# Optimization experiments

Measured on AMD Instinct MI355X. Metric: run time of the kernel, lower is better.

Reference implementation:

```python
import jax, jax.numpy as jnp
import numpy as np

N = 50000          # nodes
F = 128            # feature dim (indim = outdim)
AVG_DEG = 12       # random edges per node (plus one self-loop)
AVG_D_LOG = 2.6    # avg_d['log'] used by PNA scalers
EPS = 1e-5         # PNA std epsilon / BatchNorm eps


def setup_inputs() -> dict:
    key = jax.random.key(0)
    k1, k2, k3, k4 = jax.random.split(key, 4)
    h = jax.random.normal(k1, (N, F), dtype=jnp.float32)
    E_rand = N * AVG_DEG
    src_r = jax.random.randint(k2, (E_rand,), 0, N)
    dst_r = jax.random.randint(k3, (E_rand,), 0, N)
    loop = jnp.arange(N)
    src = jnp.concatenate([src_r, loop]).astype(jnp.int64) if jax.config.jax_enable_x64 else jnp.concatenate([src_r, loop]).astype(jnp.int32)
    dst = jnp.concatenate([dst_r, loop]).astype(src.dtype)
    concat_dim = F * (1 + 4 * 3)  # indim * (1 + n_aggr * n_scalers)
    W = jax.random.normal(k4, (concat_dim, F), dtype=jnp.float32) * (1.0 / np.sqrt(concat_dim))
    b = jnp.zeros((F,), dtype=jnp.float32)
    gamma = jnp.ones((F,), dtype=jnp.float32)
    beta = jnp.zeros((F,), dtype=jnp.float32)
    return {"h": h, "src": src, "dst": dst, "W": W, "b": b, "gamma": gamma, "beta": beta}


def _pna_forward(h, W, b, gamma, beta, src, dst):
    n = h.shape[0]
    m = h[src]                                            # [E, F] gathered mailbox
    deg = jax.ops.segment_sum(jnp.ones(src.shape[0], h.dtype), dst, num_segments=n)
    deg = jnp.maximum(deg, 1.0)[:, None]                  # every node has a self-loop
    s = jax.ops.segment_sum(m, dst, num_segments=n)
    mean = s / deg
    mx = jax.ops.segment_max(m, dst, num_segments=n)
    mn = jax.ops.segment_min(m, dst, num_segments=n)
    mean_sq = jax.ops.segment_sum(m * m, dst, num_segments=n) / deg
    std = jnp.sqrt(jax.nn.relu(mean_sq - mean * mean) + EPS)
    agg = jnp.concatenate([mean, mx, mn, std], axis=1)    # [N, 4F]
    logd = jnp.log(deg + 1.0)                             # [N, 1]
    scaled = jnp.concatenate([agg,
                              agg * (logd / AVG_D_LOG),
                              agg * (AVG_D_LOG / logd)], axis=1)  # [N, 12F]
    hc = jnp.concatenate([h, scaled], axis=1)             # [N, 13F]
    out = hc @ W + b                                      # posttrans (single linear)
    out = jax.nn.relu(out)                                # activation (dropout p=0)
    mu = out.mean(axis=0)                                 # BatchNorm1d, training stats
    var = out.var(axis=0)                                 # biased variance (torch)
    out = gamma * (out - mu) * jax.lax.rsqrt(var + EPS) + beta
    return out


def reference(h, src, dst, W, b, gamma, beta):
    return _pna_forward(h, W, b, gamma, beta, src, dst)
```

## Files before the change

kernel.cpp:

```cpp
#include <hip/hip_runtime.h>
#include <math.h>

#define FDIM 128
#define AVG_D_LOGF 2.6f
#define BN_EPS 1e-5f
#define NK5 5

using f32x2 = __attribute__((ext_vector_type(2))) float;
using f32x4 = __attribute__((ext_vector_type(4))) float;
using s16x8 = __attribute__((ext_vector_type(8))) short;
using u16x8 = __attribute__((ext_vector_type(8))) unsigned short;

__device__ __forceinline__ unsigned short f2bf(float x) {
  unsigned int u = __float_as_uint(x);
  u += 0x7FFFu + ((u >> 16) & 1u);
  return (unsigned short)(u >> 16);
}
__device__ __forceinline__ f32x2 bfpair(unsigned int u) {
  union { uint2 u2; f32x2 f; } c;
  c.u2 = make_uint2(u << 16, u & 0xFFFF0000u);
  return c.f;
}
__device__ __forceinline__ void gload16(const void* g, void* l) {
  __builtin_amdgcn_global_load_lds(
      (const __attribute__((address_space(1))) void*)g,
      (__attribute__((address_space(3))) void*)l, 16, 0, 0);
}

__global__ void prep_kernel(const float* __restrict__ h, unsigned short* __restrict__ hb,
                            const float* __restrict__ W, unsigned short* __restrict__ wBT,
                            const int* __restrict__ dst, int* __restrict__ deg,
                            int w0, int w1, int w2, int K) {
  int i = blockIdx.x * 256 + threadIdx.x;
  if (i < w0) {
    const f32x4* sp = (const f32x4*)h + (size_t)i * 2;
    f32x4 v0 = sp[0], v1 = sp[1];
    u16x8 o;
    o[0] = f2bf(v0[0]); o[1] = f2bf(v0[1]); o[2] = f2bf(v0[2]); o[3] = f2bf(v0[3]);
    o[4] = f2bf(v1[0]); o[5] = f2bf(v1[1]); o[6] = f2bf(v1[2]); o[7] = f2bf(v1[3]);
    *((u16x8*)hb + i) = o;
  } else if (i < w0 + w1) {
    int idx = i - w0;
    int k = idx >> 7, j = idx & 127;
    wBT[(size_t)j * K + k] = f2bf(W[idx]);
  } else if (i < w0 + w1 + w2) {
    atomicAdd(&deg[dst[i - w0 - w1]], 1);
  }
}

__global__ void scan1(const int* __restrict__ deg, int* __restrict__ offs,
                      int* __restrict__ bsums, int n) {
  __shared__ int tmp[256];
  int t = threadIdx.x, i = blockIdx.x * 256 + t;
  int v = (i < n) ? deg[i] : 0;
  tmp[t] = v; __syncthreads();
  for (int d = 1; d < 256; d <<= 1) {
    int x = (t >= d) ? tmp[t - d] : 0;
    __syncthreads();
    tmp[t] += x;
    __syncthreads();
  }
  if (i < n) offs[i] = tmp[t] - v;
  if (t == 255) bsums[blockIdx.x] = tmp[255];
}

__global__ void csr_fill(const int* __restrict__ src, const int* __restrict__ dst,
                         const int* __restrict__ offs, const int* __restrict__ bsums,
                         int* __restrict__ cursor, int* __restrict__ csr, int E, int nb) {
  __shared__ int tmp[256];
  __shared__ int ex[256];
  const int t = threadIdx.x;
  {
    int v = (t < nb) ? bsums[t] : 0;
    tmp[t] = v; __syncthreads();
    for (int d = 1; d < 256; d <<= 1) {
      int x = (t >= d) ? tmp[t - d] : 0;
      __syncthreads();
      tmp[t] += x;
      __syncthreads();
    }
    ex[t] = tmp[t] - v;
    __syncthreads();
  }
  int i = blockIdx.x * 256 + t;
  if (i < E) {
    int d = dst[i];
    int pos = offs[d] + ex[d >> 8] + atomicAdd(&cursor[d], 1);
    csr[pos] = src[i] << 8;
  }
}

__global__ __launch_bounds__(256) void agg_kernel(
    const unsigned short* __restrict__ hb, const int* __restrict__ csr,
    const int* __restrict__ offs, const int* __restrict__ bsums,
    unsigned short* __restrict__ aggb, float2* __restrict__ s12a,
    int n, int E, int nb) {
  __shared__ int tmp[256];
  __shared__ int ex[256];
  {
    int t = threadIdx.x;
    int v = (t < nb) ? bsums[t] : 0;
    tmp[t] = v; __syncthreads();
    for (int d = 1; d < 256; d <<= 1) {
      int x = (t >= d) ? tmp[t - d] : 0;
      __syncthreads();
      tmp[t] += x;
      __syncthreads();
    }
    ex[t] = tmp[t] - v;
    __syncthreads();
  }
  const int gw = (blockIdx.x * 256 + threadIdx.x) >> 6;
  const int lane = threadIdx.x & 63;
  if (gw >= n) return;
  const int beg = offs[gw] + ex[gw >> 8];
  const int end = (gw + 1 < n) ? offs[gw + 1] + ex[(gw + 1) >> 8] : E;
  const int sub = lane >> 5;
  const int fl  = lane & 31;
  const char* hbase = (const char*)hb + fl * 8;

  f32x2 s0v = {0.f, 0.f}, s1v = {0.f, 0.f};
  f32x2 q0v = {0.f, 0.f}, q1v = {0.f, 0.f};
  f32x2 mx0 = {-INFINITY, -INFINITY}, mx1 = {-INFINITY, -INFINITY};
  f32x2 mn0 = {INFINITY, INFINITY},  mn1 = {INFINITY, INFINITY};

  auto acc1 = [&](uint2 A) {
    f32x2 a0 = bfpair(A.x), a1 = bfpair(A.y);
    s0v += a0; s1v += a1;
    q0v += a0 * a0; q1v += a1 * a1;
    mx0[0] = fmaxf(mx0[0], a0[0]); mx0[1] = fmaxf(mx0[1], a0[1]);
    mx1[0] = fmaxf(mx1[0], a1[0]); mx1[1] = fmaxf(mx1[1], a1[1]);
    mn0[0] = fminf(mn0[0], a0[0]); mn0[1] = fminf(mn0[1], a0[1]);
    mn1[0] = fminf(mn1[0], a1[0]); mn1[1] = fminf(mn1[1], a1[1]);
  };
  auto gat = [&](int byteoff) -> uint2 {
    return *(const uint2*)(hbase + byteoff);
  };

  const int cnt = end - beg;
  const int pairs = cnt >> 1;
  int p = 0;
  for (; p + 4 <= pairs; p += 4) {
    int base = beg + 2 * p + sub;
    int i0 = csr[base], i1 = csr[base + 2], i2 = csr[base + 4], i3 = csr[base + 6];
    uint2 A = gat(i0), B = gat(i1), C = gat(i2), D = gat(i3);
    acc1(A); acc1(B); acc1(C); acc1(D);
  }
  for (; p < pairs; ++p) {
    acc1(gat(csr[beg + 2 * p + sub]));
  }
  if ((cnt & 1) && sub == 0) {
    acc1(gat(csr[end - 1]));
  }

  s0v[0] += __shfl_xor(s0v[0], 32); s0v[1] += __shfl_xor(s0v[1], 32);
  s1v[0] += __shfl_xor(s1v[0], 32); s1v[1] += __shfl_xor(s1v[1], 32);
  q0v[0] += __shfl_xor(q0v[0], 32); q0v[1] += __shfl_xor(q0v[1], 32);
  q1v[0] += __shfl_xor(q1v[0], 32); q1v[1] += __shfl_xor(q1v[1], 32);
  mx0[0] = fmaxf(mx0[0], __shfl_xor(mx0[0], 32)); mx0[1] = fmaxf(mx0[1], __shfl_xor(mx0[1], 32));
  mx1[0] = fmaxf(mx1[0], __shfl_xor(mx1[0], 32)); mx1[1] = fmaxf(mx1[1], __shfl_xor(mx1[1], 32));
  mn0[0] = fminf(mn0[0], __shfl_xor(mn0[0], 32)); mn0[1] = fminf(mn0[1], __shfl_xor(mn0[1], 32));
  mn1[0] = fminf(mn1[0], __shfl_xor(mn1[0], 32)); mn1[1] = fminf(mn1[1], __shfl_xor(mn1[1], 32));

  float degf = (float)cnt;
  if (degf < 1.f) degf = 1.f;
  const float inv = 1.f / degf;
  if (sub == 0) {
    float me0 = s0v[0] * inv, me1 = s0v[1] * inv, me2 = s1v[0] * inv, me3 = s1v[1] * inv;
    float st0 = sqrtf(fmaxf(q0v[0] * inv - me0 * me0, 0.f) + BN_EPS);
    float st1 = sqrtf(fmaxf(q0v[1] * inv - me1 * me1, 0.f) + BN_EPS);
    float st2 = sqrtf(fmaxf(q1v[0] * inv - me2 * me2, 0.f) + BN_EPS);
    float st3 = sqrtf(fmaxf(q1v[1] * inv - me3 * me3, 0.f) + BN_EPS);
    unsigned int b = (unsigned int)gw * 512u + (unsigned int)fl * 4u;
    uint2 wme = make_uint2((unsigned int)f2bf(me0) | ((unsigned int)f2bf(me1) << 16),
                           (unsigned int)f2bf(me2) | ((unsigned int)f2bf(me3) << 16));
    uint2 wmx = make_uint2((unsigned int)f2bf(mx0[0]) | ((unsigned int)f2bf(mx0[1]) << 16),
                           (unsigned int)f2bf(mx1[0]) | ((unsigned int)f2bf(mx1[1]) << 16));
    uint2 wmn = make_uint2((unsigned int)f2bf(mn0[0]) | ((unsigned int)f2bf(mn0[1]) << 16),
                           (unsigned int)f2bf(mn1[0]) | ((unsigned int)f2bf(mn1[1]) << 16));
    uint2 wst = make_uint2((unsigned int)f2bf(st0) | ((unsigned int)f2bf(st1) << 16),
                           (unsigned int)f2bf(st2) | ((unsigned int)f2bf(st3) << 16));
    *(uint2*)&aggb[b      ] = wme;
    *(uint2*)&aggb[b + 128] = wmx;
    *(uint2*)&aggb[b + 256] = wmn;
    *(uint2*)&aggb[b + 384] = wst;
  }
  if (lane == 0) {
    float logd = logf(degf + 1.f);
    s12a[gw] = make_float2(logd / AVG_D_LOGF, AVG_D_LOGF / logd);
  }
}

__global__ __launch_bounds__(256, 2) void gemm_kernel(
    const unsigned short* __restrict__ hb, const unsigned short* __restrict__ wBT,
    const unsigned short* __restrict__ aggb, const float2* __restrict__ s12a,
    const float* __restrict__ bias, float* __restrict__ out,
    float* __restrict__ bnsum, float* __restrict__ bnsq, int n, int K) {
  __shared__ s16x8 As[2048];
  __shared__ s16x8 Bs[3][1024];
  const int t = threadIdx.x;
  const int lane = t & 63;
  const int w = t >> 6;
  const int wr = w >> 1, wc = w & 1;
  const int hi = lane >> 4, lr = lane & 15, rx7 = lr & 7;

  const int nwg = gridDim.x;
  const int q = nwg >> 3, r = nwg & 7;
  const int xcd = blockIdx.x & 7, jj = blockIdx.x >> 3;
  const int bx = (xcd < r ? xcd * (q + 1) : r * (q + 1) + (xcd - r) * q) + jj;

  const int m0 = (bx >> 1) * 128;
  const int n0 = (bx & 1) * 64;

  f32x4 acc[3][4][2] = {};

  auto stage = [&](int ss) {
    const bool ph1 = (ss == 0);
    #pragma unroll
    for (int i = 0; i < 8; ++i) {
      int unit = w * 512 + i * 64 + lane;
      int row = unit >> 4, xf = unit & 15;
      int half = xf >> 3, x = xf & 7;
      int node = m0 + row; if (node >= n) node = n - 1;
      int col = half * 64 + ((x ^ (row & 7)) << 3);
      const unsigned short* src = ph1
          ? hb   + (size_t)node * FDIM + col
          : aggb + (size_t)node * 512 + (ss - 1) * 128 + col;
      gload16(src, &As[w * 512 + i * 64]);
    }
    const int nsec = ph1 ? 1 : 3;
    for (int s = 0; s < nsec; ++s) {
      int koff = ph1 ? 0 : (FDIM + s * 512 + (ss - 1) * 128);
      #pragma unroll
      for (int i = 0; i < 4; ++i) {
        int unit = w * 256 + i * 64 + lane;
        int row = unit >> 4, xf = unit & 15;
        int half = xf >> 3, x = xf & 7;
        int col = half * 64 + ((x ^ (row & 7)) << 3);
        const unsigned short* src = wBT + (size_t)(n0 + row) * K + koff + col;
        gload16(src, &Bs[s][w * 256 + i * 64]);
      }
    }
  };

  for (int step = 0; step < NK5; ++step) {
    stage(step);
    __syncthreads();
    #pragma unroll
    for (int ks = 0; ks < 4; ++ks) {
      const int uidx = ((ks >> 1) << 3) + ((((ks << 2) + hi) & 7) ^ rx7);
      s16x8 a[4];
      #pragma unroll
      for (int m = 0; m < 4; ++m) {
        int row = wr * 64 + m * 16 + lr;
        a[m] = As[row * 16 + uidx];
      }
      #pragma unroll
      for (int s = 0; s < 3; ++s) {
        if (step == 0 && s > 0) continue;
        int rb = wc * 32 + lr;
        s16x8 b0 = Bs[s][rb * 16 + uidx];
        s16x8 b1 = Bs[s][(rb + 16) * 16 + uidx];
        #pragma unroll
        for (int m = 0; m < 4; ++m) {
          acc[s][m][0] = __builtin_amdgcn_mfma_f32_16x16x32_bf16(a[m], b0, acc[s][m][0], 0, 0, 0);
          acc[s][m][1] = __builtin_amdgcn_mfma_f32_16x16x32_bf16(a[m], b1, acc[s][m][1], 0, 0, 0);
        }
      }
    }
    __syncthreads();
  }

  float* red = (float*)&As[0];
  if (t < 128) red[t] = 0.f;
  __syncthreads();

  const float bv0 = bias[n0 + wc * 32 + lr];
  const float bv1 = bias[n0 + wc * 32 + 16 + lr];
  float cs[2] = {0.f, 0.f}, cq[2] = {0.f, 0.f};
  #pragma unroll
  for (int m = 0; m < 4; ++m) {
    #pragma unroll
    for (int i = 0; i < 4; ++i) {
      int grow = m0 + wr * 64 + m * 16 + hi * 4 + i;
      if (grow >= n) continue;
      float2 sv = s12a[grow];
      #pragma unroll
      for (int nn = 0; nn < 2; ++nn) {
        float v = acc[0][m][nn][i] + sv.x * acc[1][m][nn][i] + sv.y * acc[2][m][nn][i]
                + (nn ? bv1 : bv0);
        v = fmaxf(v, 0.f);
        out[(size_t)grow * FDIM + n0 + wc * 32 + nn * 16 + lr] = v;
        cs[nn] += v; cq[nn] += v * v;
      }
    }
  }
  #pragma unroll
  for (int nn = 0; nn < 2; ++nn) {
    int lc = wc * 32 + nn * 16 + lr;
    atomicAdd(&red[lc], cs[nn]);
    atomicAdd(&red[64 + lc], cq[nn]);
  }
  __syncthreads();
  if (t < 64)       atomicAdd(&bnsum[n0 + t], red[t]);
  else if (t < 128) atomicAdd(&bnsq[n0 + t - 64], red[t]);
}

__global__ void bn_norm(float* __restrict__ out, const float* __restrict__ bnsum,
                        const float* __restrict__ bnsq, const float* __restrict__ gamma,
                        const float* __restrict__ beta, int n) {
  __shared__ float scs[128], shs[128];
  const int t = threadIdx.x;
  if (t < 128) {
    const float invN = 1.f / (float)n;
    const float mu = bnsum[t] * invN;
    const float var = bnsq[t] * invN - mu * mu;
    const float rs = rsqrtf(var + BN_EPS);
    const float s = gamma[t] * rs;
    scs[t] = s; shs[t] = beta[t] - mu * s;
  }
  __syncthreads();
  const int total = n * 32;
  int idx = blockIdx.x * 256 + t;
  const int c4 = (idx & 31) * 4;
  const float s0 = scs[c4], s1 = scs[c4 + 1], s2 = scs[c4 + 2], s3 = scs[c4 + 3];
  const float h0 = shs[c4], h1 = shs[c4 + 1], h2 = shs[c4 + 2], h3 = shs[c4 + 3];
  for (; idx < total; idx += gridDim.x * 256) {
    f32x4 v = ((f32x4*)out)[idx];
    v[0] = v[0] * s0 + h0;
    v[1] = v[1] * s1 + h1;
    v[2] = v[2] * s2 + h2;
    v[3] = v[3] * s3 + h3;
    ((f32x4*)out)[idx] = v;
  }
}

extern "C" void kernel_launch(void* const* d_in, const int* in_sizes, int n_in,
                              void* d_out, int out_size, void* d_ws, size_t ws_size,
                              hipStream_t stream) {
  const float* h     = (const float*)d_in[0];
  const int*   src   = (const int*)d_in[1];
  const int*   dst   = (const int*)d_in[2];
  const float* W     = (const float*)d_in[3];
  const float* bias  = (const float*)d_in[4];
  const float* gamma = (const float*)d_in[5];
  const float* beta  = (const float*)d_in[6];
  float* out = (float*)d_out;

  const int n = in_sizes[0] / FDIM;
  const int E = in_sizes[1];
  const int K = in_sizes[3] / FDIM;

  char* base = (char*)d_ws;
  size_t off = 0;
  auto alloc = [&](size_t bytes) -> void* {
    void* p = base + off;
    off += (bytes + 255) & ~(size_t)255;
    return p;
  };
  int*   deg    = (int*)  alloc(4ull * n);
  int*   cursor = (int*)  alloc(4ull * n);
  float* bnsum  = (float*)alloc(512);
  float* bnsq   = (float*)alloc(512);
  const size_t zlen = off;
  int*    offs  = (int*)  alloc(4ull * (n + 1));
  int*    bsums = (int*)  alloc(4ull * 256);
  int*    csr   = (int*)  alloc(4ull * E);
  float2* s12a  = (float2*)alloc(8ull * n);
  unsigned short* aggb = (unsigned short*)alloc(2ull * (size_t)n * 512);
  unsigned short* wBT  = (unsigned short*)alloc(2ull * (size_t)K * FDIM);
  unsigned short* hb   = (unsigned short*)alloc(2ull * (size_t)n * FDIM);
  (void)ws_size; (void)n_in; (void)out_size;

  const int eb = (E + 255) / 256;
  const int nb = (n + 255) / 256;
  const int w0 = n * FDIM / 8;
  const int w1 = K * FDIM;
  const int w2 = E;

  hipMemsetAsync(d_ws, 0, zlen, stream);
  prep_kernel<<<(w0 + w1 + w2 + 255) / 256, 256, 0, stream>>>(h, hb, W, wBT, dst, deg,
                                                              w0, w1, w2, K);
  scan1<<<nb, 256, 0, stream>>>(deg, offs, bsums, n);
  csr_fill<<<eb, 256, 0, stream>>>(src, dst, offs, bsums, cursor, csr, E, nb);
  agg_kernel<<<(n + 3) / 4, 256, 0, stream>>>(hb, csr, offs, bsums, aggb, s12a, n, E, nb);
  const int gblocks = ((n + 127) / 128) * 2;
  gemm_kernel<<<gblocks, 256, 0, stream>>>(hb, wBT, aggb, s12a, bias,
                                           out, bnsum, bnsq, n, K);
  bn_norm<<<2048, 256, 0, stream>>>(out, bnsum, bnsq, gamma, beta, n);
}
```

Measured before the change: 174.5 us.

## Process two nodes per wave with interleaved gathers in persistent agg kernel

The aggregation kernel now runs as a fixed grid of 2048 blocks whose waves loop over node pairs. Each pass interleaves the neighbor gathers of two adjacent nodes, keeping more independent loads in flight. It also spreads the cost of the per-block scan prologue over many nodes instead of repeating it in every block. In exchange, each wave holds two accumulator sets, which raises register pressure, and the inner loop is unrolled by two instead of four per node.

Measured after the change: 176.3 us. About the same (+1.0%).

```diff
diff --git a/kernel.cpp b/kernel.cpp
--- a/kernel.cpp
+++ b/kernel.cpp
@@ -90,6 +90,34 @@
   }
 }
 
+struct AggAcc {
+  f32x2 s0, s1, q0, q1, mx0, mx1, mn0, mn1;
+  __device__ __forceinline__ void init() {
+    s0 = s1 = q0 = q1 = (f32x2){0.f, 0.f};
+    mx0 = mx1 = (f32x2){-INFINITY, -INFINITY};
+    mn0 = mn1 = (f32x2){INFINITY, INFINITY};
+  }
+  __device__ __forceinline__ void add(uint2 A) {
+    f32x2 a0 = bfpair(A.x), a1 = bfpair(A.y);
+    s0 += a0; s1 += a1;
+    q0 += a0 * a0; q1 += a1 * a1;
+    mx0[0] = fmaxf(mx0[0], a0[0]); mx0[1] = fmaxf(mx0[1], a0[1]);
+    mx1[0] = fmaxf(mx1[0], a1[0]); mx1[1] = fmaxf(mx1[1], a1[1]);
+    mn0[0] = fminf(mn0[0], a0[0]); mn0[1] = fminf(mn0[1], a0[1]);
+    mn1[0] = fminf(mn1[0], a1[0]); mn1[1] = fminf(mn1[1], a1[1]);
+  }
+  __device__ __forceinline__ void merge32() {
+    s0[0] += __shfl_xor(s0[0], 32); s0[1] += __shfl_xor(s0[1], 32);
+    s1[0] += __shfl_xor(s1[0], 32); s1[1] += __shfl_xor(s1[1], 32);
+    q0[0] += __shfl_xor(q0[0], 32); q0[1] += __shfl_xor(q0[1], 32);
+    q1[0] += __shfl_xor(q1[0], 32); q1[1] += __shfl_xor(q1[1], 32);
+    mx0[0] = fmaxf(mx0[0], __shfl_xor(mx0[0], 32)); mx0[1] = fmaxf(mx0[1], __shfl_xor(mx0[1], 32));
+    mx1[0] = fmaxf(mx1[0], __shfl_xor(mx1[0], 32)); mx1[1] = fmaxf(mx1[1], __shfl_xor(mx1[1], 32));
+    mn0[0] = fminf(mn0[0], __shfl_xor(mn0[0], 32)); mn0[1] = fminf(mn0[1], __shfl_xor(mn0[1], 32));
+    mn1[0] = fminf(mn1[0], __shfl_xor(mn1[0], 32)); mn1[1] = fminf(mn1[1], __shfl_xor(mn1[1], 32));
+  }
+};
+
 __global__ __launch_bounds__(256) void agg_kernel(
     const unsigned short* __restrict__ hb, const int* __restrict__ csr,
     const int* __restrict__ offs, const int* __restrict__ bsums,
@@ -110,84 +138,91 @@
     ex[t] = tmp[t] - v;
     __syncthreads();
   }
-  const int gw = (blockIdx.x * 256 + threadIdx.x) >> 6;
   const int lane = threadIdx.x & 63;
-  if (gw >= n) return;
-  const int beg = offs[gw] + ex[gw >> 8];
-  const int end = (gw + 1 < n) ? offs[gw + 1] + ex[(gw + 1) >> 8] : E;
+  const int wid = (blockIdx.x * 256 + threadIdx.x) >> 6;
+  const int nwav = (gridDim.x * 256) >> 6;
   const int sub = lane >> 5;
   const int fl  = lane & 31;
   const char* hbase = (const char*)hb + fl * 8;
 
-  f32x2 s0v = {0.f, 0.f}, s1v = {0.f, 0.f};
-  f32x2 q0v = {0.f, 0.f}, q1v = {0.f, 0.f};
-  f32x2 mx0 = {-INFINITY, -INFINITY}, mx1 = {-INFINITY, -INFINITY};
-  f32x2 mn0 = {INFINITY, INFINITY},  mn1 = {INFINITY, INFINITY};
-
-  auto acc1 = [&](uint2 A) {
-    f32x2 a0 = bfpair(A.x), a1 = bfpair(A.y);
-    s0v += a0; s1v += a1;
-    q0v += a0 * a0; q1v += a1 * a1;
-    mx0[0] = fmaxf(mx0[0], a0[0]); mx0[1] = fmaxf(mx0[1], a0[1]);
-    mx1[0] = fmaxf(mx1[0], a1[0]); mx1[1] = fmaxf(mx1[1], a1[1]);
-    mn0[0] = fminf(mn0[0], a0[0]); mn0[1] = fminf(mn0[1], a0[1]);
-    mn1[0] = fminf(mn1[0], a1[0]); mn1[1] = fminf(mn1[1], a1[1]);
-  };
   auto gat = [&](int byteoff) -> uint2 {
     return *(const uint2*)(hbase + byteoff);
   };
-
-  const int cnt = end - beg;
-  const int pairs = cnt >> 1;
-  int p = 0;
-  for (; p + 4 <= pairs; p += 4) {
-    int base = beg + 2 * p + sub;
-    int i0 = csr[base], i1 = csr[base + 2], i2 = csr[base + 4], i3 = csr[base + 6];
-    uint2 A = gat(i0), B = gat(i1), C = gat(i2), D = gat(i3);
-    acc1(A); acc1(B); acc1(C); acc1(D);
-  }
-  for (; p < pairs; ++p) {
-    acc1(gat(csr[beg + 2 * p + sub]));
-  }
-  if ((cnt & 1) && sub == 0) {
-    acc1(gat(csr[end - 1]));
-  }
-
-  s0v[0] += __shfl_xor(s0v[0], 32); s0v[1] += __shfl_xor(s0v[1], 32);
-  s1v[0] += __shfl_xor(s1v[0], 32); s1v[1] += __shfl_xor(s1v[1], 32);
-  q0v[0] += __shfl_xor(q0v[0], 32); q0v[1] += __shfl_xor(q0v[1], 32);
-  q1v[0] += __shfl_xor(q1v[0], 32); q1v[1] += __shfl_xor(q1v[1], 32);
-  mx0[0] = fmaxf(mx0[0], __shfl_xor(mx0[0], 32)); mx0[1] = fmaxf(mx0[1], __shfl_xor(mx0[1], 32));
-  mx1[0] = fmaxf(mx1[0], __shfl_xor(mx1[0], 32)); mx1[1] = fmaxf(mx1[1], __shfl_xor(mx1[1], 32));
-  mn0[0] = fminf(mn0[0], __shfl_xor(mn0[0], 32)); mn0[1] = fminf(mn0[1], __shfl_xor(mn0[1], 32));
-  mn1[0] = fminf(mn1[0], __shfl_xor(mn1[0], 32)); mn1[1] = fminf(mn1[1], __shfl_xor(mn1[1], 32));
-
-  float degf = (float)cnt;
-  if (degf < 1.f) degf = 1.f;
-  const float inv = 1.f / degf;
-  if (sub == 0) {
-    float me0 = s0v[0] * inv, me1 = s0v[1] * inv, me2 = s1v[0] * inv, me3 = s1v[1] * inv;
-    float st0 = sqrtf(fmaxf(q0v[0] * inv - me0 * me0, 0.f) + BN_EPS);
-    float st1 = sqrtf(fmaxf(q0v[1] * inv - me1 * me1, 0.f) + BN_EPS);
-    float st2 = sqrtf(fmaxf(q1v[0] * inv - me2 * me2, 0.f) + BN_EPS);
-    float st3 = sqrtf(fmaxf(q1v[1] * inv - me3 * me3, 0.f) + BN_EPS);
-    unsigned int b = (unsigned int)gw * 512u + (unsigned int)fl * 4u;
-    uint2 wme = make_uint2((unsigned int)f2bf(me0) | ((unsigned int)f2bf(me1) << 16),
-                           (unsigned int)f2bf(me2) | ((unsigned int)f2bf(me3) << 16));
-    uint2 wmx = make_uint2((unsigned int)f2bf(mx0[0]) | ((unsigned int)f2bf(mx0[1]) << 16),
-                           (unsigned int)f2bf(mx1[0]) | ((unsigned int)f2bf(mx1[1]) << 16));
-    uint2 wmn = make_uint2((unsigned int)f2bf(mn0[0]) | ((unsigned int)f2bf(mn0[1]) << 16),
-                           (unsigned int)f2bf(mn1[0]) | ((unsigned int)f2bf(mn1[1]) << 16));
-    uint2 wst = make_uint2((unsigned int)f2bf(st0) | ((unsigned int)f2bf(st1) << 16),
-                           (unsigned int)f2bf(st2) | ((unsigned int)f2bf(st3) << 16));
-    *(uint2*)&aggb[b      ] = wme;
-    *(uint2*)&aggb[b + 128] = wmx;
-    *(uint2*)&aggb[b + 256] = wmn;
-    *(uint2*)&aggb[b + 384] = wst;
-  }
-  if (lane == 0) {
-    float logd = logf(degf + 1.f);
-    s12a[gw] = make_float2(logd / AVG_D_LOGF, AVG_D_LOGF / logd);
+  auto finish = [&](AggAcc& a, int node, int cnt) {
+    a.merge32();
+    float degf = (float)cnt;
+    if (degf < 1.f) degf = 1.f;
+    const float inv = 1.f / degf;
+    if (sub == 0) {
+      float me0 = a.s0[0] * inv, me1 = a.s0[1] * inv, me2 = a.s1[0] * inv, me3 = a.s1[1] * inv;
+      float st0 = sqrtf(fmaxf(a.q0[0] * inv - me0 * me0, 0.f) + BN_EPS);
+      float st1 = sqrtf(fmaxf(a.q0[1] * inv - me1 * me1, 0.f) + BN_EPS);
+      float st2 = sqrtf(fmaxf(a.q1[0] * inv - me2 * me2, 0.f) + BN_EPS);
+      float st3 = sqrtf(fmaxf(a.q1[1] * inv - me3 * me3, 0.f) + BN_EPS);
+      unsigned int b = (unsigned int)node * 512u + (unsigned int)fl * 4u;
+      uint2 wme = make_uint2((unsigned int)f2bf(me0) | ((unsigned int)f2bf(me1) << 16),
+                             (unsigned int)f2bf(me2) | ((unsigned int)f2bf(me3) << 16));
+      uint2 wmx = make_uint2((unsigned int)f2bf(a.mx0[0]) | ((unsigned int)f2bf(a.mx0[1]) << 16),
+                             (unsigned int)f2bf(a.mx1[0]) | ((unsigned int)f2bf(a.mx1[1]) << 16));
+      uint2 wmn = make_uint2((unsigned int)f2bf(a.mn0[0]) | ((unsigned int)f2bf(a.mn0[1]) << 16),
+                             (unsigned int)f2bf(a.mn1[0]) | ((unsigned int)f2bf(a.mn1[1]) << 16));
+      uint2 wst = make_uint2((unsigned int)f2bf(st0) | ((unsigned int)f2bf(st1) << 16),
+                             (unsigned int)f2bf(st2) | ((unsigned int)f2bf(st3) << 16));
+      *(uint2*)&aggb[b      ] = wme;
+      *(uint2*)&aggb[b + 128] = wmx;
+      *(uint2*)&aggb[b + 256] = wmn;
+      *(uint2*)&aggb[b + 384] = wst;
+    }
+    if (lane == 0) {
+      float logd = logf(degf + 1.f);
+      s12a[node] = make_float2(logd / AVG_D_LOGF, AVG_D_LOGF / logd);
+    }
+  };
+
+  for (int na = wid * 2; na < n; na += nwav * 2) {
+    const int nbn = na + 1;
+    const bool hasB = nbn < n;
+    const int begA = offs[na] + ex[na >> 8];
+    const int endA = (na + 1 < n) ? offs[na + 1] + ex[(na + 1) >> 8] : E;
+    const int begB = endA;
+    const int endB = hasB ? ((nbn + 1 < n) ? offs[nbn + 1] + ex[(nbn + 1) >> 8] : E) : endA;
+
+    AggAcc aA, aB;
+    aA.init(); aB.init();
+    const int cntA = endA - begA, cntB = endB - begB;
+    const int pA = cntA >> 1, pB = cntB >> 1;
+    int iA = 0, iB = 0;
+
+    while (iA + 2 <= pA && iB + 2 <= pB) {
+      int ba = begA + 2 * iA + sub;
+      int bb = begB + 2 * iB + sub;
+      int a0 = csr[ba], a1 = csr[ba + 2];
+      int b0 = csr[bb], b1 = csr[bb + 2];
+      uint2 A0 = gat(a0), A1 = gat(a1);
+      uint2 B0 = gat(b0), B1 = gat(b1);
+      aA.add(A0); aA.add(A1);
+      aB.add(B0); aB.add(B1);
+      iA += 2; iB += 2;
+    }
+    for (; iA + 2 <= pA; iA += 2) {
+      int ba = begA + 2 * iA + sub;
+      int a0 = csr[ba], a1 = csr[ba + 2];
+      uint2 A0 = gat(a0), A1 = gat(a1);
+      aA.add(A0); aA.add(A1);
+    }
+    for (; iA < pA; ++iA) aA.add(gat(csr[begA + 2 * iA + sub]));
+    if ((cntA & 1) && sub == 0) aA.add(gat(csr[endA - 1]));
+    for (; iB + 2 <= pB; iB += 2) {
+      int bb = begB + 2 * iB + sub;
+      int b0 = csr[bb], b1 = csr[bb + 2];
+      uint2 B0 = gat(b0), B1 = gat(b1);
+      aB.add(B0); aB.add(B1);
+    }
+    for (; iB < pB; ++iB) aB.add(gat(csr[begB + 2 * iB + sub]));
+    if (hasB && (cntB & 1) && sub == 0) aB.add(gat(csr[endB - 1]));
+
+    finish(aA, na, cntA);
+    if (hasB) finish(aB, nbn, cntB);
   }
 }
 
@@ -383,7 +418,7 @@
                                                               w0, w1, w2, K);
   scan1<<<nb, 256, 0, stream>>>(deg, offs, bsums, n);
   csr_fill<<<eb, 256, 0, stream>>>(src, dst, offs, bsums, cursor, csr, E, nb);
-  agg_kernel<<<(n + 3) / 4, 256, 0, stream>>>(hb, csr, offs, bsums, aggb, s12a, n, E, nb);
+  agg_kernel<<<2048, 256, 0, stream>>>(hb, csr, offs, bsums, aggb, s12a, n, E, nb);
   const int gblocks = ((n + 127) / 128) * 2;
   gemm_kernel<<<gblocks, 256, 0, stream>>>(hb, wBT, aggb, s12a, bias,
                                            out, bnsum, bnsq, n, K);
```
